# Kernel optimization log

Hardware: AMD Instinct MI355X
Metric: run time of the kernel (lower is better)

Reference implementation:

```python
import jax, jax.numpy as jnp
import numpy as np

N = 100000   # nodes
E = 1600000  # edges
H = 128      # hidden_dim
B = 4096     # number of root pairs
HOPS = 3


def setup_inputs() -> dict:
    key = jax.random.key(0)
    ks = jax.random.split(key, 12)
    s = 0.05
    return {
        "node_feat": jax.random.normal(ks[0], (N, H), jnp.float32),
        "send_embd": jax.random.normal(ks[1], (N, H), jnp.float32),
        "edge_index": jax.random.randint(ks[2], (2, E), 0, N, dtype=jnp.int32),
        "root_index": jax.random.randint(ks[3], (2 * B,), 0, N, dtype=jnp.int32),
        "agg_by_source": 1,
        "lin1_W": jax.random.normal(ks[4], (2 * H, H), jnp.float32) * s,
        "lin1_b": jnp.zeros((H,), jnp.float32),
        "gat_W": jax.random.normal(ks[5], (HOPS, H, H), jnp.float32) * s,
        "gat_asrc": jax.random.normal(ks[6], (HOPS, H), jnp.float32) * s,
        "gat_adst": jax.random.normal(ks[7], (HOPS, H), jnp.float32) * s,
        "gat_b": jnp.zeros((HOPS, H), jnp.float32),
        "lstm_Wih": jax.random.normal(ks[8], (HOPS, 2 * H, 4 * H), jnp.float32) * s,
        "lstm_Whh": jax.random.normal(ks[9], (HOPS, H, 4 * H), jnp.float32) * s,
        "lstm_b": jnp.zeros((HOPS, 4 * H), jnp.float32),
        "lin2_W": jax.random.normal(ks[10], (H, H), jnp.float32) * s,
        "lin2_b": jnp.zeros((H,), jnp.float32),
    }


def _gat_breadth(x, src, dst, W, a_src, a_dst, b):
    # GATConv(heads=1) followed by tanh (GeniePath Breadth layer)
    xw = x @ W                                  # [N, H]
    e_score = jax.nn.leaky_relu((xw @ a_src)[src] + (xw @ a_dst)[dst], 0.2)  # [E]
    # softmax over incoming edges of each destination node
    m = jax.ops.segment_max(e_score, dst, num_segments=N)
    ex = jnp.exp(e_score - m[dst])
    z = jax.ops.segment_sum(ex, dst, num_segments=N)
    alpha = ex / z[dst]                          # [E]
    agg = jax.ops.segment_sum(alpha[:, None] * xw[src], dst, num_segments=N)
    return jnp.tanh(agg + b)


def _lstm_step(inp, h, c, Wih, Whh, b):
    gates = inp @ Wih + h @ Whh + b              # [N, 4H]
    i, f, g, o = jnp.split(gates, 4, axis=-1)
    c = jax.nn.sigmoid(f) * c + jax.nn.sigmoid(i) * jnp.tanh(g)
    h = jax.nn.sigmoid(o) * jnp.tanh(c)
    return h, c


def reference(node_feat, send_embd, edge_index, root_index, agg_by_source,
              lin1_W, lin1_b, gat_W, gat_asrc, gat_adst, gat_b,
              lstm_Wih, lstm_Whh, lstm_b, lin2_W, lin2_b):
    src, dst = edge_index[0], edge_index[1]
    # Aggregation stage input: concat node embedding with broadcast embedding
    x = jnp.concatenate([node_feat, send_embd], axis=1) @ lin1_W + lin1_b  # [N, H]
    # GeniePathLazy: all breadth (GAT) layers run on the projected input x
    h_tmps = [
        _gat_breadth(x, src, dst, gat_W[i], gat_asrc[i], gat_adst[i], gat_b[i])
        for i in range(HOPS)
    ]
    # Depth: per-node LSTM over the hop axis, input = cat(h_tmp, x_prev)
    h = jnp.zeros_like(x)
    c = jnp.zeros_like(x)
    xs = x
    for i in range(HOPS):
        inp = jnp.concatenate([h_tmps[i], xs], axis=1)   # [N, 2H]
        h, c = _lstm_step(inp, h, c, lstm_Wih[i], lstm_Whh[i], lstm_b[i])
        xs = h
    out = xs @ lin2_W + lin2_b                            # [N, H]
    roots = root_index.reshape(-1, 2)
    src_nodes = roots[:, 0] if agg_by_source else roots[:, 1]
    return out[src_nodes]                                 # [B, H]
```

## Files before the change

### kernel.cpp

```cpp
#include <hip/hip_runtime.h>

constexpr int N  = 100000;
constexpr int E  = 1600000;
constexpr int H  = 128;
constexpr int NB = 4096;
constexpr int HOPS = 3;
constexpr int EPT = 8;

constexpr int WOFF_L1  = 0;
constexpr int WOFF_GAT = 32768;
constexpr int WOFF_CAT = 81920;
constexpr int WOFF_L2  = 671744;
constexpr int WTOT     = 688128;

constexpr size_t ALIGN = 256;
constexpr size_t alup(size_t x) { return (x + ALIGN - 1) & ~(ALIGN - 1); }

constexpr size_t OFF_X       = 0;
constexpr size_t OFF_SSRC    = alup(OFF_X + (size_t)N * H * 4);
constexpr size_t OFF_SDST    = alup(OFF_SSRC + (size_t)3 * N * 4);
constexpr size_t OFF_WVEC    = alup(OFF_SDST + (size_t)3 * N * 4);
constexpr size_t OFF_SELMAP  = alup(OFF_WVEC + 6 * H * 4);
constexpr size_t OFF_NODELST = alup(OFF_SELMAP + (size_t)N * 4);
constexpr size_t OFF_CNT     = alup(OFF_NODELST + NB * 4);
constexpr size_t OFF_DEG     = alup(OFF_CNT + 256);
constexpr size_t OFF_OFFS    = alup(OFF_DEG + NB * 4);
constexpr size_t OFF_CURSOR  = alup(OFF_OFFS + (NB + 1) * 4);
constexpr size_t OFF_ESORT   = alup(OFF_CURSOR + NB * 4);
constexpr size_t OFF_AGGXH   = alup(OFF_ESORT + (size_t)E * 4);
constexpr size_t OFF_AGGXL   = alup(OFF_AGGXH + (size_t)3 * NB * H * 2);
constexpr size_t OFF_XSH     = alup(OFF_AGGXL + (size_t)3 * NB * H * 2);
constexpr size_t OFF_XSL     = alup(OFF_XSH + (size_t)NB * H * 2);
constexpr size_t OFF_HH      = alup(OFF_XSL + (size_t)NB * H * 2);
constexpr size_t OFF_HL      = alup(OFF_HH + (size_t)NB * H * 2);
constexpr size_t OFF_CBUF    = alup(OFF_HL + (size_t)NB * H * 2);
constexpr size_t OFF_L2OUT   = alup(OFF_CBUF + (size_t)NB * H * 4);
constexpr size_t OFF_WHI     = alup(OFF_L2OUT + (size_t)NB * H * 4);
constexpr size_t OFF_WLO     = alup(OFF_WHI + (size_t)WTOT * 2);

__device__ __forceinline__ float lrelu(float v) { return v > 0.f ? v : 0.2f * v; }
__device__ __forceinline__ float sigmoidf_(float v) { return 1.f / (1.f + __expf(-v)); }

__device__ __forceinline__ unsigned short f2bf(float f) {
  unsigned u = __float_as_uint(f);
  unsigned r = (u + 0x7FFFu + ((u >> 16) & 1u)) >> 16;
  return (unsigned short)r;
}
__device__ __forceinline__ float bf2f(unsigned short h) {
  return __uint_as_float((unsigned)h << 16);
}
__device__ __forceinline__ void split_rne(float f, unsigned short& hi, unsigned short& lo) {
  unsigned short hh = f2bf(f);
  hi = hh;
  lo = f2bf(f - bf2f(hh));
}
__device__ __forceinline__ void split_trunc(float f, short* hi, short* lo) {
  unsigned u = __float_as_uint(f);
  *hi = (short)(u >> 16);
  float r = f - __uint_as_float(u & 0xFFFF0000u);
  *lo = (short)(__float_as_uint(r) >> 16);
}

typedef short bf16x8 __attribute__((ext_vector_type(8)));
typedef float f32x4  __attribute__((ext_vector_type(4)));

#define MFMA3(ACC, AH, AL, BH, BL)                                               \
  ACC = __builtin_amdgcn_mfma_f32_16x16x32_bf16(AH, BH, ACC, 0, 0, 0);           \
  ACC = __builtin_amdgcn_mfma_f32_16x16x32_bf16(AH, BL, ACC, 0, 0, 0);           \
  ACC = __builtin_amdgcn_mfma_f32_16x16x32_bf16(AL, BH, ACC, 0, 0, 0);

__global__ void init_ws(int* __restrict__ sel_map, int* __restrict__ deg,
                        int* __restrict__ cursor, int* __restrict__ cnt,
                        float* __restrict__ cbuf, unsigned short* __restrict__ hh,
                        unsigned short* __restrict__ hl, int* __restrict__ need_flag) {
  int i = blockIdx.x * 256 + threadIdx.x;
  int stride = gridDim.x * 256;
  for (int n = i; n < N; n += stride) { sel_map[n] = -1; need_flag[n] = 0; }
  for (int n = i; n < NB; n += stride) { deg[n] = 0; cursor[n] = 0; }
  if (i < 64) cnt[i] = 0;
  for (int n = i; n < NB * H; n += stride) { cbuf[n] = 0.f; hh[n] = 0; hl[n] = 0; }
}

__global__ void prep_kernel(const float* __restrict__ gat_W,
                            const float* __restrict__ a_src,
                            const float* __restrict__ a_dst,
                            float* __restrict__ wvec,
                            const float* __restrict__ lin1_W,
                            const float* __restrict__ Wih,
                            const float* __restrict__ Whh,
                            const float* __restrict__ lin2_W,
                            unsigned short* __restrict__ whi,
                            unsigned short* __restrict__ wlo) {
  if (blockIdx.x < 6) {
    int i = blockIdx.x >> 1, which = blockIdx.x & 1;
    int k = threadIdx.x;
    __shared__ float av[H];
    if (k < H) av[k] = which ? a_dst[i * H + k] : a_src[i * H + k];
    __syncthreads();
    if (k >= H) return;
    const float* Wr = gat_W + (size_t)i * H * H + (size_t)k * H;
    float s = 0.f;
    #pragma unroll 8
    for (int j = 0; j < H; j++) s = fmaf(Wr[j], av[j], s);
    wvec[(i * 2 + which) * H + k] = s;
    return;
  }
  int idx = (blockIdx.x - 6) * 256 + threadIdx.x;
  if (idx >= WTOT) return;
  float v;
  if (idx < WOFF_GAT) {
    int rel = idx;
    int e = rel & 7, lane = (rel >> 3) & 63, tile = rel >> 9;
    int nl = lane & 15, quad = lane >> 4;
    int c = tile & 7, t = tile >> 3;
    int n = c * 16 + nl, k = t * 32 + quad * 8 + e;
    v = lin1_W[k * 128 + n];
  } else if (idx < WOFF_CAT) {
    int rel = idx - WOFF_GAT;
    int hop = rel / 16384; rel %= 16384;
    int e = rel & 7, lane = (rel >> 3) & 63, tile = rel >> 9;
    int nl = lane & 15, quad = lane >> 4;
    int c = tile & 7, t = tile >> 3;
    int n = c * 16 + nl, k = t * 32 + quad * 8 + e;
    v = gat_W[hop * 16384 + k * 128 + n];
  } else if (idx < WOFF_L2) {
    int rel = idx - WOFF_CAT;
    int hop = rel / 196608; rel %= 196608;
    int e = rel & 7, lane = (rel >> 3) & 63, tile = rel >> 9;
    int nl = lane & 15, quad = lane >> 4;
    int c = tile & 31, t = tile >> 5;
    int ftile = c >> 2, g = c & 3;
    int col = g * 128 + ftile * 16 + nl;
    int k = t * 32 + quad * 8 + e;
    v = (k < 256) ? Wih[hop * 131072 + k * 512 + col]
                  : Whh[hop * 65536 + (k - 256) * 512 + col];
  } else {
    int rel = idx - WOFF_L2;
    int e = rel & 7, lane = (rel >> 3) & 63, tile = rel >> 9;
    int nl = lane & 15, quad = lane >> 4;
    int c = tile & 7, t = tile >> 3;
    int n = c * 16 + nl, k = t * 32 + quad * 8 + e;
    v = lin2_W[k * 128 + n];
  }
  unsigned short hh, ll;
  split_rne(v, hh, ll);
  whi[idx] = hh;
  wlo[idx] = ll;
}

__global__ void roots_assign(const int* __restrict__ root, const int* __restrict__ aggp,
                             int* __restrict__ sel_map, int* __restrict__ node_list,
                             int* __restrict__ cnt, int* __restrict__ need_flag) {
  int b = blockIdx.x * 256 + threadIdx.x;
  if (b >= NB) return;
  int node = root[2 * b + (aggp[0] ? 0 : 1)];
  need_flag[node] = 1;
  int old = atomicCAS(&sel_map[node], -1, -2);
  if (old == -1) {
    int c = atomicAdd(cnt, 1);
    sel_map[node] = c;
    node_list[c] = node;
  }
}

__global__ void count_edges(const int* __restrict__ ei, const int* __restrict__ sel_map,
                            int* __restrict__ deg) {
  const int T = gridDim.x * 256;
  const int base = blockIdx.x * 256 + threadIdx.x;
  int dn[EPT];
  #pragma unroll
  for (int k = 0; k < EPT; k++) {
    int e = base + k * T;
    dn[k] = (e < E) ? ei[E + e] : -1;
  }
  #pragma unroll
  for (int k = 0; k < EPT; k++) {
    if (dn[k] >= 0) dn[k] = sel_map[dn[k]];
  }
  #pragma unroll
  for (int k = 0; k < EPT; k++) {
    if (dn[k] >= 0) atomicAdd(&deg[dn[k]], 1);
  }
}

__global__ __launch_bounds__(1024)
void scan_kernel(const int* __restrict__ deg, int* __restrict__ offs) {
  __shared__ int part[1024];
  int t = threadIdx.x;
  int base = t * 4;
  int v0 = deg[base], v1 = deg[base + 1], v2 = deg[base + 2], v3 = deg[base + 3];
  int s = v0 + v1 + v2 + v3;
  part[t] = s;
  __syncthreads();
  for (int off = 1; off < 1024; off <<= 1) {
    int tmp = (t >= off) ? part[t - off] : 0;
    __syncthreads();
    part[t] += tmp;
    __syncthreads();
  }
  int run = part[t] - s;
  offs[base] = run; run += v0;
  offs[base + 1] = run; run += v1;
  offs[base + 2] = run; run += v2;
  offs[base + 3] = run;
  if (t == 1023) offs[NB] = part[1023];
}

__global__ void scatter_edges2(const int* __restrict__ ei, const int* __restrict__ sel_map,
                               const int* __restrict__ offs, int* __restrict__ cursor,
                               int* __restrict__ es_sorted, int* __restrict__ need_flag) {
  const int T = gridDim.x * 256;
  const int base = blockIdx.x * 256 + threadIdx.x;
  int dn[EPT], sn[EPT];
  #pragma unroll
  for (int k = 0; k < EPT; k++) {
    int e = base + k * T;
    dn[k] = (e < E) ? ei[E + e] : -1;
  }
  #pragma unroll
  for (int k = 0; k < EPT; k++) {
    if (dn[k] >= 0) dn[k] = sel_map[dn[k]];
  }
  #pragma unroll
  for (int k = 0; k < EPT; k++) {
    int e = base + k * T;
    if (dn[k] >= 0) sn[k] = ei[e];
  }
  #pragma unroll
  for (int k = 0; k < EPT; k++) {
    if (dn[k] >= 0) {
      int p = atomicAdd(&cursor[dn[k]], 1);
      es_sorted[offs[dn[k]] + p] = sn[k];
      need_flag[sn[k]] = 1;
    }
  }
}

__global__ void compact_need(const int* __restrict__ need_flag,
                             int* __restrict__ need_list, int* __restrict__ need_cnt) {
  int i = blockIdx.x * 256 + threadIdx.x;
  bool f = (i < N) && (need_flag[i] != 0);
  unsigned long long mask = __ballot(f);
  int lane = threadIdx.x & 63;
  int wcnt = __popcll(mask);
  int base = 0;
  if (lane == 0 && wcnt > 0) base = atomicAdd(need_cnt, wcnt);
  base = __shfl(base, 0);
  if (f) {
    int prefix = __popcll(mask & ((1ull << lane) - 1ull));
    need_list[base + prefix] = i;
  }
}

__global__ __launch_bounds__(256)
void gemm_lin1(const float* __restrict__ a0, const float* __restrict__ a1,
               const unsigned short* __restrict__ Bth,
               const unsigned short* __restrict__ Btl,
               const float* __restrict__ bias, float* __restrict__ Cc,
               const float* __restrict__ wvec,
               float* __restrict__ s_src, float* __restrict__ s_dst,
               const int* __restrict__ need_list, const int* __restrict__ need_cnt) {
  const int t = threadIdx.x, lane = t & 63, wave = t >> 6;
  const int nl = lane & 15, quad = lane >> 4;
  const int nneed = need_cnt[0];
  if (blockIdx.x * 64 >= nneed) return;
  const int rt = blockIdx.x * 64 + wave * 16;

  int gr = rt + nl;
  const int rowi = (gr < nneed) ? need_list[gr] : -1;

  float4 va[8][2];
  #pragma unroll
  for (int kt = 0; kt < 8; kt++) {
    const float* A = (kt < 4) ? a0 : a1;
    const int kk = (kt & 3) * 32 + quad * 8;
    float4 v0 = make_float4(0.f, 0.f, 0.f, 0.f), v1 = v0;
    if (rowi >= 0) {
      const float* p = A + (size_t)rowi * H + kk;
      v0 = *(const float4*)p;
      v1 = *(const float4*)(p + 4);
    }
    va[kt][0] = v0;
    va[kt][1] = v1;
  }

  f32x4 acc[8];
  #pragma unroll
  for (int c = 0; c < 8; c++) acc[c] = (f32x4){0.f, 0.f, 0.f, 0.f};

  #pragma unroll
  for (int kt = 0; kt < 8; kt++) {
    bf16x8 ahi, alo;
    {
      float4 v0 = va[kt][0], v1 = va[kt][1];
      float af[8] = {v0.x, v0.y, v0.z, v0.w, v1.x, v1.y, v1.z, v1.w};
      #pragma unroll
      for (int j = 0; j < 8; j++) {
        short h_, l_;
        split_trunc(af[j], &h_, &l_);
        ahi[j] = h_;
        alo[j] = l_;
      }
    }
    #pragma unroll
    for (int c = 0; c < 8; c++) {
      size_t boff = ((size_t)(kt * 8 + c) * 64 + lane) * 8;
      bf16x8 bh = *(const bf16x8*)(Bth + boff);
      bf16x8 bl = *(const bf16x8*)(Btl + boff);
      MFMA3(acc[c], ahi, alo, bh, bl);
    }
  }

  float bv[8], wvf[6][8];
  #pragma unroll
  for (int c = 0; c < 8; c++) {
    int col = c * 16 + nl;
    bv[c] = bias[col];
    #pragma unroll
    for (int v6 = 0; v6 < 6; v6++) wvf[v6][c] = wvec[v6 * 128 + col];
  }
  #pragma unroll
  for (int r = 0; r < 4; r++) {
    int gr2 = rt + quad * 4 + r;
    if (gr2 >= nneed) continue;
    int row = need_list[gr2];
    float* cr = Cc + (size_t)row * H;
    float sc[6] = {0.f, 0.f, 0.f, 0.f, 0.f, 0.f};
    #pragma unroll
    for (int c = 0; c < 8; c++) {
      float val = acc[c][r] + bv[c];
      cr[c * 16 + nl] = val;
      #pragma unroll
      for (int v6 = 0; v6 < 6; v6++) sc[v6] = fmaf(val, wvf[v6][c], sc[v6]);
    }
    #pragma unroll
    for (int m = 1; m < 16; m <<= 1)
      #pragma unroll
      for (int v6 = 0; v6 < 6; v6++) sc[v6] += __shfl_xor(sc[v6], m);
    if (nl == 0) {
      #pragma unroll
      for (int h3 = 0; h3 < 3; h3++) {
        s_src[h3 * N + row] = sc[2 * h3 + 0];
        s_dst[h3 * N + row] = sc[2 * h3 + 1];
      }
    }
  }
}

__global__ __launch_bounds__(128)
void gat_node_kernel(const int* __restrict__ node_list, const int* __restrict__ cntp,
                     const int* __restrict__ offs, const int* __restrict__ es_sorted,
                     const float* __restrict__ x, const float* __restrict__ s_src,
                     const float* __restrict__ s_dst,
                     unsigned short* __restrict__ aggxh, unsigned short* __restrict__ aggxl,
                     unsigned short* __restrict__ xsh, unsigned short* __restrict__ xsl) {
  int c = blockIdx.x;
  if (c >= cntp[0]) return;
  int t = threadIdx.x;
  int n = node_list[c];
  {
    float xv = x[(size_t)n * H + t];
    unsigned short vh, vl;
    split_rne(xv, vh, vl);
    xsh[(size_t)c * H + t] = vh;
    xsl[(size_t)c * H + t] = vl;
  }
  float sd0 = s_dst[0 * N + n], sd1 = s_dst[1 * N + n], sd2 = s_dst[2 * N + n];
  int e0 = offs[c], e1 = offs[c + 1];
  float m0 = -1e30f, m1 = -1e30f, m2 = -1e30f;
  for (int e = e0 + t; e < e1; e += 128) {
    int s = es_sorted[e];
    m0 = fmaxf(m0, lrelu(s_src[0 * N + s] + sd0));
    m1 = fmaxf(m1, lrelu(s_src[1 * N + s] + sd1));
    m2 = fmaxf(m2, lrelu(s_src[2 * N + s] + sd2));
  }
  __shared__ float red[3][128];
  red[0][t] = m0; red[1][t] = m1; red[2][t] = m2;
  __syncthreads();
  for (int s2 = 64; s2 > 0; s2 >>= 1) {
    if (t < s2) {
      red[0][t] = fmaxf(red[0][t], red[0][t + s2]);
      red[1][t] = fmaxf(red[1][t], red[1][t + s2]);
      red[2][t] = fmaxf(red[2][t], red[2][t + s2]);
    }
    __syncthreads();
  }
  m0 = red[0][0]; m1 = red[1][0]; m2 = red[2][0];
  float u0 = 0.f, u1 = 0.f, u2 = 0.f, z0 = 0.f, z1 = 0.f, z2 = 0.f;
  for (int e = e0; e < e1; e++) {
    int s = es_sorted[e];
    float xs = x[(size_t)s * H + t];
    float ex0 = __expf(lrelu(s_src[0 * N + s] + sd0) - m0);
    float ex1 = __expf(lrelu(s_src[1 * N + s] + sd1) - m1);
    float ex2 = __expf(lrelu(s_src[2 * N + s] + sd2) - m2);
    z0 += ex0; z1 += ex1; z2 += ex2;
    u0 = fmaf(ex0, xs, u0); u1 = fmaf(ex1, xs, u1); u2 = fmaf(ex2, xs, u2);
  }
  size_t cb = (size_t)c * H + t;
  bool any = e1 > e0;
  float v0 = any ? u0 / z0 : 0.f;
  float v1 = any ? u1 / z1 : 0.f;
  float v2 = any ? u2 / z2 : 0.f;
  unsigned short vh, vl;
  split_rne(v0, vh, vl); aggxh[0 * ((size_t)NB * H) + cb] = vh; aggxl[0 * ((size_t)NB * H) + cb] = vl;
  split_rne(v1, vh, vl); aggxh[1 * ((size_t)NB * H) + cb] = vh; aggxl[1 * ((size_t)NB * H) + cb] = vl;
  split_rne(v2, vh, vl); aggxh[2 * ((size_t)NB * H) + cb] = vh; aggxl[2 * ((size_t)NB * H) + cb] = vl;
}

__global__ __launch_bounds__(256)
void hop_fused(const unsigned short* __restrict__ agh, const unsigned short* __restrict__ agl,
               const unsigned short* __restrict__ gWh, const unsigned short* __restrict__ gWl,
               const float* __restrict__ gbias,
               const unsigned short* __restrict__ x1h, const unsigned short* __restrict__ x1l,
               const unsigned short* __restrict__ CWh, const unsigned short* __restrict__ CWl,
               const float* __restrict__ lbias,
               float* __restrict__ cbuf, unsigned short* __restrict__ hh,
               unsigned short* __restrict__ hl,
               const unsigned short* __restrict__ L2h, const unsigned short* __restrict__ L2l,
               const float* __restrict__ lin2_b, float* __restrict__ l2out, int do_lin2) {
  __shared__ unsigned short Hh[16 * 136];
  __shared__ unsigned short Hl[16 * 136];
  const int t = threadIdx.x, lane = t & 63, wave = t >> 6;
  const int nl = lane & 15, quad = lane >> 4;
  const int r0 = blockIdx.x * 16;

  f32x4 acc1[2];
  #pragma unroll
  for (int j = 0; j < 2; j++) acc1[j] = (f32x4){0.f, 0.f, 0.f, 0.f};
  #pragma unroll
  for (int kt = 0; kt < 4; kt++) {
    size_t aoff = (size_t)(r0 + nl) * H + kt * 32 + quad * 8;
    bf16x8 ah = *(const bf16x8*)(agh + aoff);
    bf16x8 al = *(const bf16x8*)(agl + aoff);
    #pragma unroll
    for (int j = 0; j < 2; j++) {
      size_t boff = ((size_t)(kt * 8 + 2 * wave + j) * 64 + lane) * 8;
      bf16x8 bh = *(const bf16x8*)(gWh + boff);
      bf16x8 bl = *(const bf16x8*)(gWl + boff);
      MFMA3(acc1[j], ah, al, bh, bl);
    }
  }
  #pragma unroll
  for (int j = 0; j < 2; j++) {
    int col = wave * 32 + j * 16 + nl;
    float bv = gbias[col];
    #pragma unroll
    for (int r = 0; r < 4; r++) {
      int rl = quad * 4 + r;
      float v = tanhf(acc1[j][r] + bv);
      unsigned short vh, vl2;
      split_rne(v, vh, vl2);
      Hh[rl * 136 + col] = vh;
      Hl[rl * 136 + col] = vl2;
    }
  }
  __syncthreads();

  f32x4 acc2[8];
  #pragma unroll
  for (int j = 0; j < 8; j++) acc2[j] = (f32x4){0.f, 0.f, 0.f, 0.f};
  for (int kt = 0; kt < 12; kt++) {
    int kk = (kt & 3) * 32 + quad * 8;
    bf16x8 ah, al;
    if (kt < 4) {
      ah = *(const bf16x8*)&Hh[nl * 136 + kk];
      al = *(const bf16x8*)&Hl[nl * 136 + kk];
    } else {
      const unsigned short* ph = (kt < 8) ? x1h : hh;
      const unsigned short* pl = (kt < 8) ? x1l : hl;
      size_t aoff = (size_t)(r0 + nl) * H + kk;
      ah = *(const bf16x8*)(ph + aoff);
      al = *(const bf16x8*)(pl + aoff);
    }
    #pragma unroll
    for (int cc = 0; cc < 8; cc++) {
      size_t boff = ((size_t)(kt * 32 + 8 * wave + cc) * 64 + lane) * 8;
      bf16x8 bh = *(const bf16x8*)(CWh + boff);
      bf16x8 bl = *(const bf16x8*)(CWl + boff);
      MFMA3(acc2[cc], ah, al, bh, bl);
    }
  }
  __syncthreads();

  #pragma unroll
  for (int ft = 0; ft < 2; ft++) {
    int f = (2 * wave + ft) * 16 + nl;
    float b_i = lbias[0 * 128 + f], b_f = lbias[1 * 128 + f];
    float b_g = lbias[2 * 128 + f], b_o = lbias[3 * 128 + f];
    #pragma unroll
    for (int r = 0; r < 4; r++) {
      int rl = quad * 4 + r;
      size_t id = (size_t)(r0 + rl) * H + f;
      float gi = acc2[ft * 4 + 0][r] + b_i;
      float gf = acc2[ft * 4 + 1][r] + b_f;
      float gg = acc2[ft * 4 + 2][r] + b_g;
      float go = acc2[ft * 4 + 3][r] + b_o;
      float cp = cbuf[id];
      float cn = sigmoidf_(gf) * cp + sigmoidf_(gi) * tanhf(gg);
      float hn = sigmoidf_(go) * tanhf(cn);
      cbuf[id] = cn;
      unsigned short vh, vl2;
      split_rne(hn, vh, vl2);
      hh[id] = vh;
      hl[id] = vl2;
      if (do_lin2) { Hh[rl * 136 + f] = vh; Hl[rl * 136 + f] = vl2; }
    }
  }

  if (!do_lin2) return;
  __syncthreads();
  f32x4 acc3[2];
  #pragma unroll
  for (int j = 0; j < 2; j++) acc3[j] = (f32x4){0.f, 0.f, 0.f, 0.f};
  #pragma unroll
  for (int kt = 0; kt < 4; kt++) {
    int kk = kt * 32 + quad * 8;
    bf16x8 ah = *(const bf16x8*)&Hh[nl * 136 + kk];
    bf16x8 al = *(const bf16x8*)&Hl[nl * 136 + kk];
    #pragma unroll
    for (int j = 0; j < 2; j++) {
      size_t boff = ((size_t)(kt * 8 + 2 * wave + j) * 64 + lane) * 8;
      bf16x8 bh = *(const bf16x8*)(L2h + boff);
      bf16x8 bl = *(const bf16x8*)(L2l + boff);
      MFMA3(acc3[j], ah, al, bh, bl);
    }
  }
  #pragma unroll
  for (int j = 0; j < 2; j++) {
    int col = wave * 32 + j * 16 + nl;
    float bv = lin2_b[col];
    #pragma unroll
    for (int r = 0; r < 4; r++) {
      int row = r0 + quad * 4 + r;
      l2out[(size_t)row * H + col] = acc3[j][r] + bv;
    }
  }
}

__global__ void scatter_out(const float* __restrict__ l2out, const int* __restrict__ sel_map,
                            const int* __restrict__ root, const int* __restrict__ aggp,
                            float* __restrict__ out) {
  int id = blockIdx.x * 256 + threadIdx.x;
  if (id >= NB * H) return;
  int b = id >> 7, f = id & 127;
  int node = root[2 * b + (aggp[0] ? 0 : 1)];
  int c = sel_map[node];
  out[id] = l2out[(size_t)c * H + f];
}

extern "C" void kernel_launch(void* const* d_in, const int* in_sizes, int n_in,
                              void* d_out, int out_size, void* d_ws, size_t ws_size,
                              hipStream_t stream) {
  const float* node_feat = (const float*)d_in[0];
  const float* send_embd = (const float*)d_in[1];
  const int*   edge_idx  = (const int*)d_in[2];
  const int*   root_idx  = (const int*)d_in[3];
  const int*   aggp      = (const int*)d_in[4];
  const float* lin1_W    = (const float*)d_in[5];
  const float* lin1_b    = (const float*)d_in[6];
  const float* gat_W     = (const float*)d_in[7];
  const float* gat_asrc  = (const float*)d_in[8];
  const float* gat_adst  = (const float*)d_in[9];
  const float* gat_b     = (const float*)d_in[10];
  const float* lstm_Wih  = (const float*)d_in[11];
  const float* lstm_Whh  = (const float*)d_in[12];
  const float* lstm_b    = (const float*)d_in[13];
  const float* lin2_W    = (const float*)d_in[14];
  const float* lin2_b    = (const float*)d_in[15];
  float* out = (float*)d_out;

  char* ws = (char*)d_ws;
  float* x       = (float*)(ws + OFF_X);
  float* s_src   = (float*)(ws + OFF_SSRC);
  float* s_dst   = (float*)(ws + OFF_SDST);
  float* wvec    = (float*)(ws + OFF_WVEC);
  int*   sel_map = (int*)(ws + OFF_SELMAP);
  int*   nodelst = (int*)(ws + OFF_NODELST);
  int*   cnt     = (int*)(ws + OFF_CNT);
  int*   deg     = (int*)(ws + OFF_DEG);
  int*   offs    = (int*)(ws + OFF_OFFS);
  int*   cursor  = (int*)(ws + OFF_CURSOR);
  int*   esort   = (int*)(ws + OFF_ESORT);
  unsigned short* aggxh = (unsigned short*)(ws + OFF_AGGXH);
  unsigned short* aggxl = (unsigned short*)(ws + OFF_AGGXL);
  unsigned short* xsh   = (unsigned short*)(ws + OFF_XSH);
  unsigned short* xsl   = (unsigned short*)(ws + OFF_XSL);
  unsigned short* hh    = (unsigned short*)(ws + OFF_HH);
  unsigned short* hl    = (unsigned short*)(ws + OFF_HL);
  float* cbuf    = (float*)(ws + OFF_CBUF);
  float* l2out   = (float*)(ws + OFF_L2OUT);
  unsigned short* whi = (unsigned short*)(ws + OFF_WHI);
  unsigned short* wlo = (unsigned short*)(ws + OFF_WLO);

  int* need_flag = (int*)(ws + OFF_AGGXH);
  int* need_list = need_flag + N;
  int* need_cnt  = cnt + 1;

  init_ws<<<2048, 256, 0, stream>>>(sel_map, deg, cursor, cnt, cbuf, hh, hl, need_flag);
  prep_kernel<<<6 + (WTOT + 255) / 256, 256, 0, stream>>>(
      gat_W, gat_asrc, gat_adst, wvec, lin1_W, lstm_Wih, lstm_Whh, lin2_W, whi, wlo);
  roots_assign<<<(NB + 255) / 256, 256, 0, stream>>>(root_idx, aggp, sel_map, nodelst, cnt,
                                                     need_flag);

  const int egrid = (E + 256 * EPT - 1) / (256 * EPT);
  count_edges<<<egrid, 256, 0, stream>>>(edge_idx, sel_map, deg);
  scan_kernel<<<1, 1024, 0, stream>>>(deg, offs);
  scatter_edges2<<<egrid, 256, 0, stream>>>(edge_idx, sel_map, offs, cursor, esort,
                                            need_flag);
  compact_need<<<(N + 255) / 256, 256, 0, stream>>>(need_flag, need_list, need_cnt);

  gemm_lin1<<<(N + 63) / 64, 256, 0, stream>>>(
      node_feat, send_embd, whi + WOFF_L1, wlo + WOFF_L1, lin1_b, x,
      wvec, s_src, s_dst, need_list, need_cnt);

  gat_node_kernel<<<NB, 128, 0, stream>>>(nodelst, cnt, offs, esort, x, s_src, s_dst,
                                          aggxh, aggxl, xsh, xsl);

  for (int i = 0; i < HOPS; i++) {
    const unsigned short* x1h = (i == 0) ? xsh : hh;
    const unsigned short* x1l = (i == 0) ? xsl : hl;
    hop_fused<<<NB / 16, 256, 0, stream>>>(
        aggxh + (size_t)i * NB * H, aggxl + (size_t)i * NB * H,
        whi + WOFF_GAT + i * 16384, wlo + WOFF_GAT + i * 16384,
        gat_b + (size_t)i * H,
        x1h, x1l,
        whi + WOFF_CAT + i * 196608, wlo + WOFF_CAT + i * 196608,
        lstm_b + (size_t)i * 512,
        cbuf, hh, hl,
        whi + WOFF_L2, wlo + WOFF_L2, lin2_b, l2out,
        (i == HOPS - 1) ? 1 : 0);
  }

  scatter_out<<<(NB * H + 255) / 256, 256, 0, stream>>>(l2out, sel_map, root_idx, aggp, out);
}
```

Measured before the change: 379.7 us.

## Fold lin1 into GAT scores and aggregate raw inputs before projecting

Attention scores are now computed straight from the raw 256-wide concatenated inputs using precomputed folded vectors (lin1_W·wvec plus a bias constant). This replaces the full lin1 GEMM over every needed node with a cheap dot-product pass. Because aggregation is linear, softmax aggregation runs over raw 256-wide features, and lin1 is applied afterwards only to the 4096×3 aggregated rows plus the root rows in a single unified GEMM. The trade-off is that the gather now reads twice as many bytes per edge, and a different rounding order could change numerics slightly.

After: 387.1 us. About the same (+1.9%).

```diff
diff --git a/kernel.cpp b/kernel.cpp
--- a/kernel.cpp
+++ b/kernel.cpp
@@ -37,6 +37,10 @@
 constexpr size_t OFF_L2OUT   = alup(OFF_CBUF + (size_t)NB * H * 4);
 constexpr size_t OFF_WHI     = alup(OFF_L2OUT + (size_t)NB * H * 4);
 constexpr size_t OFF_WLO     = alup(OFF_WHI + (size_t)WTOT * 2);
+
+constexpr size_t OFF_AGGRAW  = OFF_X;
+constexpr size_t OFF_WV2     = OFF_X + (size_t)16 * 1024 * 1024;
+constexpr size_t OFF_C2      = OFF_WV2 + 6 * 256 * 4;
 
 __device__ __forceinline__ float lrelu(float v) { return v > 0.f ? v : 0.2f * v; }
 __device__ __forceinline__ float sigmoidf_(float v) { return 1.f / (1.f + __expf(-v)); }
@@ -148,6 +152,27 @@
   wlo[idx] = ll;
 }
 
+__global__ void prep2_kernel(const float* __restrict__ lin1_W,
+                             const float* __restrict__ lin1_b,
+                             const float* __restrict__ wvec,
+                             float* __restrict__ wv2, float* __restrict__ c2) {
+  int v = blockIdx.x;
+  int j = threadIdx.x;
+  __shared__ float wv[H];
+  if (j < H) wv[j] = wvec[v * H + j];
+  __syncthreads();
+  const float* Wr = lin1_W + (size_t)j * H;
+  float s = 0.f;
+  #pragma unroll 8
+  for (int m = 0; m < H; m++) s = fmaf(Wr[m], wv[m], s);
+  wv2[v * 256 + j] = s;
+  if (j == 0) {
+    float cc = 0.f;
+    for (int m = 0; m < H; m++) cc = fmaf(lin1_b[m], wv[m], cc);
+    c2[v] = cc;
+  }
+}
+
 __global__ void roots_assign(const int* __restrict__ root, const int* __restrict__ aggp,
                              int* __restrict__ sel_map, int* __restrict__ node_list,
                              int* __restrict__ cnt, int* __restrict__ need_flag) {
@@ -253,46 +278,142 @@
 }
 
 __global__ __launch_bounds__(256)
-void gemm_lin1(const float* __restrict__ a0, const float* __restrict__ a1,
-               const unsigned short* __restrict__ Bth,
-               const unsigned short* __restrict__ Btl,
-               const float* __restrict__ bias, float* __restrict__ Cc,
-               const float* __restrict__ wvec,
-               float* __restrict__ s_src, float* __restrict__ s_dst,
-               const int* __restrict__ need_list, const int* __restrict__ need_cnt) {
+void score_pass(const float* __restrict__ a0, const float* __restrict__ a1,
+                const float* __restrict__ wv2, const float* __restrict__ c2,
+                float* __restrict__ s_src, float* __restrict__ s_dst,
+                const int* __restrict__ need_list, const int* __restrict__ need_cnt) {
+  const int nneed = need_cnt[0];
+  if (blockIdx.x * 16 >= nneed) return;
+  __shared__ float Ws[6 * 256];
+  __shared__ float C2s[6];
+  const int t = threadIdx.x, lane = t & 63, wave = t >> 6;
+  const int nl = lane & 15;
+  #pragma unroll
+  for (int v = 0; v < 6; v++) Ws[v * 256 + t] = wv2[v * 256 + t];
+  if (t < 6) C2s[t] = c2[t];
+  __syncthreads();
+
+  int r = blockIdx.x * 16 + wave * 4 + (lane >> 4);
+  int row = (r < nneed) ? need_list[r] : -1;
+  int rc = (row < 0) ? 0 : row;
+  const float* src = (nl < 8) ? (a0 + (size_t)rc * H + nl * 16)
+                              : (a1 + (size_t)rc * H + (nl - 8) * 16);
+  float4 va[4];
+  #pragma unroll
+  for (int q = 0; q < 4; q++) va[q] = ((const float4*)src)[q];
+
+  float p[6] = {0.f, 0.f, 0.f, 0.f, 0.f, 0.f};
+  #pragma unroll
+  for (int q = 0; q < 4; q++) {
+    float4 v4 = va[q];
+    #pragma unroll
+    for (int v = 0; v < 6; v++) {
+      float4 w4 = *(const float4*)&Ws[v * 256 + nl * 16 + q * 4];
+      p[v] = fmaf(v4.x, w4.x, p[v]);
+      p[v] = fmaf(v4.y, w4.y, p[v]);
+      p[v] = fmaf(v4.z, w4.z, p[v]);
+      p[v] = fmaf(v4.w, w4.w, p[v]);
+    }
+  }
+  #pragma unroll
+  for (int m = 1; m < 16; m <<= 1)
+    #pragma unroll
+    for (int v = 0; v < 6; v++) p[v] += __shfl_xor(p[v], m);
+  if (nl == 0 && row >= 0) {
+    #pragma unroll
+    for (int h3 = 0; h3 < 3; h3++) {
+      s_src[h3 * N + row] = p[2 * h3 + 0] + C2s[2 * h3 + 0];
+      s_dst[h3 * N + row] = p[2 * h3 + 1] + C2s[2 * h3 + 1];
+    }
+  }
+}
+
+__global__ __launch_bounds__(256)
+void gat_node_kernel(const int* __restrict__ node_list, const int* __restrict__ cntp,
+                     const int* __restrict__ offs, const int* __restrict__ es_sorted,
+                     const float* __restrict__ a0, const float* __restrict__ a1,
+                     const float* __restrict__ s_src, const float* __restrict__ s_dst,
+                     float* __restrict__ agg_raw) {
+  int c = blockIdx.x;
+  if (c >= cntp[0]) return;
+  int t = threadIdx.x;
+  int n = node_list[c];
+  float sd0 = s_dst[0 * N + n], sd1 = s_dst[1 * N + n], sd2 = s_dst[2 * N + n];
+  int e0 = offs[c], e1 = offs[c + 1];
+  float m0 = -1e30f, m1 = -1e30f, m2 = -1e30f;
+  for (int e = e0 + t; e < e1; e += 256) {
+    int s = es_sorted[e];
+    m0 = fmaxf(m0, lrelu(s_src[0 * N + s] + sd0));
+    m1 = fmaxf(m1, lrelu(s_src[1 * N + s] + sd1));
+    m2 = fmaxf(m2, lrelu(s_src[2 * N + s] + sd2));
+  }
+  __shared__ float red[3][256];
+  red[0][t] = m0; red[1][t] = m1; red[2][t] = m2;
+  __syncthreads();
+  for (int s2 = 128; s2 > 0; s2 >>= 1) {
+    if (t < s2) {
+      red[0][t] = fmaxf(red[0][t], red[0][t + s2]);
+      red[1][t] = fmaxf(red[1][t], red[1][t + s2]);
+      red[2][t] = fmaxf(red[2][t], red[2][t + s2]);
+    }
+    __syncthreads();
+  }
+  m0 = red[0][0]; m1 = red[1][0]; m2 = red[2][0];
+  float u0 = 0.f, u1 = 0.f, u2 = 0.f, z0 = 0.f, z1 = 0.f, z2 = 0.f;
+  for (int e = e0; e < e1; e++) {
+    int s = es_sorted[e];
+    float xs = (t < 128) ? a0[(size_t)s * H + t] : a1[(size_t)s * H + (t - 128)];
+    float ex0 = __expf(lrelu(s_src[0 * N + s] + sd0) - m0);
+    float ex1 = __expf(lrelu(s_src[1 * N + s] + sd1) - m1);
+    float ex2 = __expf(lrelu(s_src[2 * N + s] + sd2) - m2);
+    z0 += ex0; z1 += ex1; z2 += ex2;
+    u0 = fmaf(ex0, xs, u0); u1 = fmaf(ex1, xs, u1); u2 = fmaf(ex2, xs, u2);
+  }
+  size_t cb = (size_t)c * 256 + t;
+  bool any = e1 > e0;
+  agg_raw[0 * ((size_t)NB * 256) + cb] = any ? u0 / z0 : 0.f;
+  agg_raw[1 * ((size_t)NB * 256) + cb] = any ? u1 / z1 : 0.f;
+  agg_raw[2 * ((size_t)NB * 256) + cb] = any ? u2 / z2 : 0.f;
+}
+
+__global__ __launch_bounds__(256)
+void gemm_unified(const float* __restrict__ agg_raw,
+                  const float* __restrict__ a0, const float* __restrict__ a1,
+                  const int* __restrict__ node_list, const int* __restrict__ cntp,
+                  const int* __restrict__ offs,
+                  const unsigned short* __restrict__ Bth,
+                  const unsigned short* __restrict__ Btl,
+                  const float* __restrict__ bias,
+                  unsigned short* __restrict__ aggxh, unsigned short* __restrict__ aggxl,
+                  unsigned short* __restrict__ xsh, unsigned short* __restrict__ xsl) {
   const int t = threadIdx.x, lane = t & 63, wave = t >> 6;
   const int nl = lane & 15, quad = lane >> 4;
-  const int nneed = need_cnt[0];
-  if (blockIdx.x * 64 >= nneed) return;
   const int rt = blockIdx.x * 64 + wave * 16;
+  const int cnt = cntp[0];
 
   int gr = rt + nl;
-  const int rowi = (gr < nneed) ? need_list[gr] : -1;
-
-  float4 va[8][2];
+  const float *pA, *pB;
+  if (gr < 12288) {
+    pA = agg_raw + (size_t)gr * 256;
+    pB = pA + 128;
+  } else {
+    int cc = gr - 12288;
+    int node = (cc < cnt) ? node_list[cc] : 0;
+    pA = a0 + (size_t)node * H;
+    pB = a1 + (size_t)node * H;
+  }
+
+  f32x4 acc[8];
+  #pragma unroll
+  for (int c = 0; c < 8; c++) acc[c] = (f32x4){0.f, 0.f, 0.f, 0.f};
+
   #pragma unroll
   for (int kt = 0; kt < 8; kt++) {
-    const float* A = (kt < 4) ? a0 : a1;
-    const int kk = (kt & 3) * 32 + quad * 8;
-    float4 v0 = make_float4(0.f, 0.f, 0.f, 0.f), v1 = v0;
-    if (rowi >= 0) {
-      const float* p = A + (size_t)rowi * H + kk;
-      v0 = *(const float4*)p;
-      v1 = *(const float4*)(p + 4);
-    }
-    va[kt][0] = v0;
-    va[kt][1] = v1;
-  }
-
-  f32x4 acc[8];
-  #pragma unroll
-  for (int c = 0; c < 8; c++) acc[c] = (f32x4){0.f, 0.f, 0.f, 0.f};
-
-  #pragma unroll
-  for (int kt = 0; kt < 8; kt++) {
+    const float* p = ((kt < 4) ? pA : pB) + (kt & 3) * 32 + quad * 8;
     bf16x8 ahi, alo;
     {
-      float4 v0 = va[kt][0], v1 = va[kt][1];
+      float4 v0 = *(const float4*)p;
+      float4 v1 = *(const float4*)(p + 4);
       float af[8] = {v0.x, v0.y, v0.z, v0.w, v1.x, v1.y, v1.z, v1.w};
       #pragma unroll
       for (int j = 0; j < 8; j++) {
@@ -311,100 +432,38 @@
     }
   }
 
-  float bv[8], wvf[6][8];
-  #pragma unroll
-  for (int c = 0; c < 8; c++) {
-    int col = c * 16 + nl;
-    bv[c] = bias[col];
-    #pragma unroll
-    for (int v6 = 0; v6 < 6; v6++) wvf[v6][c] = wvec[v6 * 128 + col];
-  }
+  float bv[8];
+  #pragma unroll
+  for (int c = 0; c < 8; c++) bv[c] = bias[c * 16 + nl];
+
   #pragma unroll
   for (int r = 0; r < 4; r++) {
-    int gr2 = rt + quad * 4 + r;
-    if (gr2 >= nneed) continue;
-    int row = need_list[gr2];
-    float* cr = Cc + (size_t)row * H;
-    float sc[6] = {0.f, 0.f, 0.f, 0.f, 0.f, 0.f};
-    #pragma unroll
-    for (int c = 0; c < 8; c++) {
-      float val = acc[c][r] + bv[c];
-      cr[c * 16 + nl] = val;
+    int g2 = rt + quad * 4 + r;
+    if (g2 < 12288) {
+      int cc = g2 & 4095, h = g2 >> 12;
+      bool he = offs[cc + 1] > offs[cc];
+      size_t base = (size_t)h * NB * H + (size_t)cc * H;
       #pragma unroll
-      for (int v6 = 0; v6 < 6; v6++) sc[v6] = fmaf(val, wvf[v6][c], sc[v6]);
-    }
-    #pragma unroll
-    for (int m = 1; m < 16; m <<= 1)
+      for (int c = 0; c < 8; c++) {
+        float val = acc[c][r] + (he ? bv[c] : 0.f);
+        unsigned short vh, vl;
+        split_rne(val, vh, vl);
+        aggxh[base + c * 16 + nl] = vh;
+        aggxl[base + c * 16 + nl] = vl;
+      }
+    } else {
+      int cc = g2 - 12288;
+      size_t base = (size_t)cc * H;
       #pragma unroll
-      for (int v6 = 0; v6 < 6; v6++) sc[v6] += __shfl_xor(sc[v6], m);
-    if (nl == 0) {
-      #pragma unroll
-      for (int h3 = 0; h3 < 3; h3++) {
-        s_src[h3 * N + row] = sc[2 * h3 + 0];
-        s_dst[h3 * N + row] = sc[2 * h3 + 1];
+      for (int c = 0; c < 8; c++) {
+        float val = acc[c][r] + bv[c];
+        unsigned short vh, vl;
+        split_rne(val, vh, vl);
+        xsh[base + c * 16 + nl] = vh;
+        xsl[base + c * 16 + nl] = vl;
       }
     }
   }
-}
-
-__global__ __launch_bounds__(128)
-void gat_node_kernel(const int* __restrict__ node_list, const int* __restrict__ cntp,
-                     const int* __restrict__ offs, const int* __restrict__ es_sorted,
-                     const float* __restrict__ x, const float* __restrict__ s_src,
-                     const float* __restrict__ s_dst,
-                     unsigned short* __restrict__ aggxh, unsigned short* __restrict__ aggxl,
-                     unsigned short* __restrict__ xsh, unsigned short* __restrict__ xsl) {
-  int c = blockIdx.x;
-  if (c >= cntp[0]) return;
-  int t = threadIdx.x;
-  int n = node_list[c];
-  {
-    float xv = x[(size_t)n * H + t];
-    unsigned short vh, vl;
-    split_rne(xv, vh, vl);
-    xsh[(size_t)c * H + t] = vh;
-    xsl[(size_t)c * H + t] = vl;
-  }
-  float sd0 = s_dst[0 * N + n], sd1 = s_dst[1 * N + n], sd2 = s_dst[2 * N + n];
-  int e0 = offs[c], e1 = offs[c + 1];
-  float m0 = -1e30f, m1 = -1e30f, m2 = -1e30f;
-  for (int e = e0 + t; e < e1; e += 128) {
-    int s = es_sorted[e];
-    m0 = fmaxf(m0, lrelu(s_src[0 * N + s] + sd0));
-    m1 = fmaxf(m1, lrelu(s_src[1 * N + s] + sd1));
-    m2 = fmaxf(m2, lrelu(s_src[2 * N + s] + sd2));
-  }
-  __shared__ float red[3][128];
-  red[0][t] = m0; red[1][t] = m1; red[2][t] = m2;
-  __syncthreads();
-  for (int s2 = 64; s2 > 0; s2 >>= 1) {
-    if (t < s2) {
-      red[0][t] = fmaxf(red[0][t], red[0][t + s2]);
-      red[1][t] = fmaxf(red[1][t], red[1][t + s2]);
-      red[2][t] = fmaxf(red[2][t], red[2][t + s2]);
-    }
-    __syncthreads();
-  }
-  m0 = red[0][0]; m1 = red[1][0]; m2 = red[2][0];
-  float u0 = 0.f, u1 = 0.f, u2 = 0.f, z0 = 0.f, z1 = 0.f, z2 = 0.f;
-  for (int e = e0; e < e1; e++) {
-    int s = es_sorted[e];
-    float xs = x[(size_t)s * H + t];
-    float ex0 = __expf(lrelu(s_src[0 * N + s] + sd0) - m0);
-    float ex1 = __expf(lrelu(s_src[1 * N + s] + sd1) - m1);
-    float ex2 = __expf(lrelu(s_src[2 * N + s] + sd2) - m2);
-    z0 += ex0; z1 += ex1; z2 += ex2;
-    u0 = fmaf(ex0, xs, u0); u1 = fmaf(ex1, xs, u1); u2 = fmaf(ex2, xs, u2);
-  }
-  size_t cb = (size_t)c * H + t;
-  bool any = e1 > e0;
-  float v0 = any ? u0 / z0 : 0.f;
-  float v1 = any ? u1 / z1 : 0.f;
-  float v2 = any ? u2 / z2 : 0.f;
-  unsigned short vh, vl;
-  split_rne(v0, vh, vl); aggxh[0 * ((size_t)NB * H) + cb] = vh; aggxl[0 * ((size_t)NB * H) + cb] = vl;
-  split_rne(v1, vh, vl); aggxh[1 * ((size_t)NB * H) + cb] = vh; aggxl[1 * ((size_t)NB * H) + cb] = vl;
-  split_rne(v2, vh, vl); aggxh[2 * ((size_t)NB * H) + cb] = vh; aggxl[2 * ((size_t)NB * H) + cb] = vl;
 }
 
 __global__ __launch_bounds__(256)
@@ -570,7 +629,9 @@
   float* out = (float*)d_out;
 
   char* ws = (char*)d_ws;
-  float* x       = (float*)(ws + OFF_X);
+  float* agg_raw = (float*)(ws + OFF_AGGRAW);
+  float* wv2     = (float*)(ws + OFF_WV2);
+  float* c2      = (float*)(ws + OFF_C2);
   float* s_src   = (float*)(ws + OFF_SSRC);
   float* s_dst   = (float*)(ws + OFF_SDST);
   float* wvec    = (float*)(ws + OFF_WVEC);
@@ -599,6 +660,7 @@
   init_ws<<<2048, 256, 0, stream>>>(sel_map, deg, cursor, cnt, cbuf, hh, hl, need_flag);
   prep_kernel<<<6 + (WTOT + 255) / 256, 256, 0, stream>>>(
       gat_W, gat_asrc, gat_adst, wvec, lin1_W, lstm_Wih, lstm_Whh, lin2_W, whi, wlo);
+  prep2_kernel<<<6, 256, 0, stream>>>(lin1_W, lin1_b, wvec, wv2, c2);
   roots_assign<<<(NB + 255) / 256, 256, 0, stream>>>(root_idx, aggp, sel_map, nodelst, cnt,
                                                      need_flag);
 
@@ -609,12 +671,16 @@
                                             need_flag);
   compact_need<<<(N + 255) / 256, 256, 0, stream>>>(need_flag, need_list, need_cnt);
 
-  gemm_lin1<<<(N + 63) / 64, 256, 0, stream>>>(
-      node_feat, send_embd, whi + WOFF_L1, wlo + WOFF_L1, lin1_b, x,
-      wvec, s_src, s_dst, need_list, need_cnt);
-
-  gat_node_kernel<<<NB, 128, 0, stream>>>(nodelst, cnt, offs, esort, x, s_src, s_dst,
-                                          aggxh, aggxl, xsh, xsl);
+  score_pass<<<(N + 15) / 16, 256, 0, stream>>>(
+      node_feat, send_embd, wv2, c2, s_src, s_dst, need_list, need_cnt);
+
+  gat_node_kernel<<<NB, 256, 0, stream>>>(nodelst, cnt, offs, esort,
+                                          node_feat, send_embd, s_src, s_dst, agg_raw);
+
+  gemm_unified<<<256, 256, 0, stream>>>(
+      agg_raw, node_feat, send_embd, nodelst, cnt, offs,
+      whi + WOFF_L1, wlo + WOFF_L1, lin1_b,
+      aggxh, aggxl, xsh, xsl);
 
   for (int i = 0; i < HOPS; i++) {
     const unsigned short* x1h = (i == 0) ? xsh : hh;
```
